# Optimization experiments

Hardware: AMD Instinct MI355X
Metric: run time of the kernel (lower is better)

Reference implementation:

```python
import jax, jax.numpy as jnp
import numpy as np

B, C, H, W, K = 16, 64, 256, 256, 3

def setup_inputs() -> dict:
    key = jax.random.key(0)
    ks = jax.random.split(key, 3)
    x = jax.random.normal(ks[0], (B, C, H, W), dtype=jnp.float32)
    # ReDistribution params
    rd_k = jnp.ones((1, C, 1, 1), jnp.float32)
    rd_b = jnp.zeros((1, C, 1, 1), jnp.float32)
    # Spectral binary activation beta
    beta = jnp.ones((1,), jnp.float32)
    # HardBinaryConv real-valued latent weights (Conv2d default init scale)
    fan_in = C * K * K
    bound = 1.0 / np.sqrt(fan_in)
    conv_w = jax.random.uniform(ks[1], (C, C, K, K), jnp.float32, -bound, bound)
    # RPReLU params
    pr_bias0 = jnp.zeros((1, C, 1, 1), jnp.float32)
    prelu_w = jnp.full((C,), 0.25, jnp.float32)
    pr_bias1 = jnp.zeros((1, C, 1, 1), jnp.float32)
    return {"x": x, "rd_k": rd_k, "rd_b": rd_b, "beta": beta,
            "conv_w": conv_w, "pr_bias0": pr_bias0, "prelu_w": prelu_w,
            "pr_bias1": pr_bias1}

def _ste(hard, soft):
    # straight-through estimator: forward=hard, backward grads flow via soft
    return jax.lax.stop_gradient(hard - soft) + soft

def reference(x, rd_k, rd_b, beta, conv_w, pr_bias0, prelu_w, pr_bias1):
    sg = jax.lax.stop_gradient
    # ReDistribution
    out = x * rd_k + rd_b
    # Spectral binary activation with tanh STE
    out = _ste(jnp.sign(out), jnp.tanh(out * beta))
    # HardBinaryConv: per-output-channel mean |w| scaling, sign binarize, clip STE
    scaling = sg(jnp.mean(jnp.abs(conv_w), axis=(1, 2, 3), keepdims=True))  # [C,1,1,1]
    bw = _ste(scaling * jnp.sign(conv_w), jnp.clip(conv_w, -1.0, 1.0))
    y = jax.lax.conv_general_dilated(
        out, bw, window_strides=(1, 1), padding=((1, 1), (1, 1)),
        dimension_numbers=("NCHW", "OIHW", "NCHW"))
    # RPReLU: bias0 -> per-channel PReLU -> bias1
    y = y + pr_bias0
    y = jnp.where(y >= 0, y, prelu_w[None, :, None, None] * y)
    y = y + pr_bias1
    return y + x
```

## Files before the change

### kernel.cpp

```cpp
#include <hip/hip_runtime.h>
#include <cstdint>
#include <cstddef>

#define Bn 16
#define Cn 64
#define Hn 256
#define Wn 256
#define HWn (Hn * Wn)
#define PIX (Bn * HWn)

#define TH 8
#define TW 64
#define NBLK (Wn / TW * Hn / TH * Bn)

__global__ __launch_bounds__(64) void pack_weights(const float* __restrict__ w,
                                                   const float* __restrict__ b0g,
                                                   const float* __restrict__ pwg,
                                                   const float* __restrict__ b1g,
                                                   uint64_t* __restrict__ wbits,
                                                   float4* __restrict__ par,
                                                   int* __restrict__ corr) {
    const int co = blockIdx.x;
    const int ci = threadIdx.x;
    const float* wp = w + ((size_t)co * Cn + ci) * 9;
    float v[9];
    float asum = 0.f;
    #pragma unroll
    for (int t = 0; t < 9; ++t) { v[t] = wp[t]; asum += fabsf(v[t]); }
    uint64_t m[9];
    #pragma unroll
    for (int t = 0; t < 9; ++t) m[t] = __ballot(v[t] > 0.f);
    #pragma unroll
    for (int off = 32; off; off >>= 1) asum += __shfl_xor(asum, off);
    if (ci == 0) {
        #pragma unroll
        for (int t = 0; t < 9; ++t) {
            wbits[co * 9 + t] = m[t];
            corr[co * 9 + t]  = 64 - 2 * (int)__popcll(m[t]);
        }
        par[co] = make_float4(asum * (1.f / (Cn * 9)), b0g[co], pwg[co], b1g[co]);
    }
}

__global__ __launch_bounds__(256, 4) void fused(const float* __restrict__ x,
                                                const float* __restrict__ rdk,
                                                const float* __restrict__ rdb,
                                                const uint64_t* __restrict__ wbits,
                                                const float4* __restrict__ par,
                                                const int* __restrict__ corr,
                                                float* __restrict__ out) {
    __shared__ uint64_t s_a[TH + 2][TW + 2];
    __shared__ float4 s_par[Cn];
    __shared__ float2 s_rd[Cn];

    const int tid = threadIdx.x;

    const int hw_id   = blockIdx.x;
    const int logical = (hw_id & 7) * (NBLK / 8) + (hw_id >> 3);
    const int w0 = (logical & 3) * TW;
    const int h0 = ((logical >> 2) & 31) * TH;
    const int n  = logical >> 7;

    if (tid < Cn) {
        s_par[tid] = par[tid];
        s_rd[tid]  = make_float2(rdk[tid], rdb[tid]);
    }
    __syncthreads();

    const float* xn = x + (size_t)n * Cn * HWn;
    for (int task = tid; task < 340; task += 256) {
        if (task < 320) {
            const int r  = task >> 5;
            const int pp = task & 31;
            const int gh = h0 - 1 + r;
            const int gw = w0 + pp * 2;
            uint64_t b0 = 0, b1 = 0;
            if (gh >= 0 && gh < Hn) {
                const float* xp = xn + (size_t)gh * Wn + gw;
                #pragma unroll 8
                for (int ci = 0; ci < Cn; ++ci) {
                    const float2 v = *reinterpret_cast<const float2*>(xp + (size_t)ci * HWn);
                    const float2 kb = s_rd[ci];
                    const uint64_t bit = 1ull << ci;
                    if (fmaf(v.x, kb.x, kb.y) > 0.f) b0 |= bit;
                    if (fmaf(v.y, kb.x, kb.y) > 0.f) b1 |= bit;
                }
            }
            s_a[r][1 + 2 * pp] = b0;
            s_a[r][2 + 2 * pp] = b1;
        } else {
            const int t2 = task - 320;
            const int r = t2 >> 1;
            const int side = t2 & 1;
            const int gh = h0 - 1 + r;
            const int gw = side ? (w0 + TW) : (w0 - 1);
            uint64_t b = 0;
            if (gh >= 0 && gh < Hn && gw >= 0 && gw < Wn) {
                const float* xp = xn + (size_t)gh * Wn + gw;
                #pragma unroll 8
                for (int ci = 0; ci < Cn; ++ci) {
                    const float v = xp[(size_t)ci * HWn];
                    const float2 kb = s_rd[ci];
                    if (fmaf(v, kb.x, kb.y) > 0.f) b |= 1ull << ci;
                }
            }
            s_a[r][side ? (TW + 1) : 0] = b;
        }
    }
    __syncthreads();

    const int lane = tid & 63;
    const int co_base = __builtin_amdgcn_readfirstlane((tid >> 6) * 16);
    const int w = w0 + lane;
    const unsigned cmask = (w == 0) ? 0x49u : (w == Wn - 1 ? 0x124u : 0u);
    const int any_edge = (w0 == 0) | (w0 + TW == Wn) | (h0 == 0) | (h0 + TH == Hn);

    uint64_t A[TH + 2][3];
    #pragma unroll
    for (int r = 0; r < TH + 2; ++r)
        #pragma unroll
        for (int dw = 0; dw < 3; ++dw)
            A[r][dw] = s_a[r][lane + dw];

    const size_t base_n = (size_t)n * Cn * HWn + (size_t)h0 * Wn + w;

    for (int c2 = 0; c2 < 8; ++c2) {
        const int coA = co_base + c2 * 2;
        const uint64_t* wbp = wbits + (size_t)coA * 9;
        uint64_t wba[9], wbb[9];
        #pragma unroll
        for (int t = 0; t < 9; ++t) { wba[t] = wbp[t]; wbb[t] = wbp[9 + t]; }
        const float4 pA = s_par[coA];
        const float4 pB = s_par[coA + 1];

        const float* xpc = x + base_n + (size_t)coA * HWn;
        float* opc = out + base_n + (size_t)coA * HWn;
        float xv[16];
        #pragma unroll
        for (int j = 0; j < 2; ++j)
            #pragma unroll
            for (int rr = 0; rr < TH; ++rr)
                xv[j * 8 + rr] = xpc[(size_t)j * HWn + (size_t)rr * Wn];

        #pragma unroll
        for (int r = 0; r < TH; ++r) {
            int accA = 0, accB = 0;
            #pragma unroll
            for (int dh = 0; dh < 3; ++dh)
                #pragma unroll
                for (int dw = 0; dw < 3; ++dw) {
                    accA += (int)__popcll(A[r + dh][dw] ^ wba[dh * 3 + dw]);
                    accB += (int)__popcll(A[r + dh][dw] ^ wbb[dh * 3 + dw]);
                }
            int isumA = 576 - 2 * accA;
            int isumB = 576 - 2 * accB;

            if (any_edge) {
                const int h = h0 + r;
                const unsigned imask = cmask |
                    ((h == 0) ? 0x7u : (h == Hn - 1 ? 0x1C0u : 0u));
                if (__any((int)imask)) {
                    #pragma unroll
                    for (int t = 0; t < 9; ++t)
                        if (imask & (1u << t)) {
                            isumA -= corr[coA * 9 + t];
                            isumB -= corr[(coA + 1) * 9 + t];
                        }
                }
            }

            float yA = fmaf(pA.x, (float)isumA, pA.y);
            yA = (yA >= 0.f) ? yA : yA * pA.z;
            yA += pA.w;
            float yB = fmaf(pB.x, (float)isumB, pB.y);
            yB = (yB >= 0.f) ? yB : yB * pB.z;
            yB += pB.w;
            opc[(size_t)r * Wn]       = yA + xv[r];
            opc[HWn + (size_t)r * Wn] = yB + xv[8 + r];
        }
    }
}

extern "C" void kernel_launch(void* const* d_in, const int* in_sizes, int n_in,
                              void* d_out, int out_size, void* d_ws, size_t ws_size,
                              hipStream_t stream) {
    const float* x      = (const float*)d_in[0];
    const float* rd_k   = (const float*)d_in[1];
    const float* rd_b   = (const float*)d_in[2];
    const float* conv_w = (const float*)d_in[4];
    const float* pb0    = (const float*)d_in[5];
    const float* pw     = (const float*)d_in[6];
    const float* pb1    = (const float*)d_in[7];
    float* out = (float*)d_out;

    uint8_t* ws = (uint8_t*)d_ws;
    uint64_t* wbits = (uint64_t*)ws;
    float4*   par   = (float4*)(ws + 4608);
    int*      corr  = (int*)(ws + 4608 + 1024);

    pack_weights<<<Cn, 64, 0, stream>>>(conv_w, pb0, pw, pb1, wbits, par, corr);
    fused<<<NBLK, 256, 0, stream>>>(x, rd_k, rd_b, wbits, par, corr, out);
}
```

Before: 199.8 us.

## Replace XNOR-popcount binary conv with int8 MFMA on ±1 activations

The binarized activations are now staged in shared memory as ±1 int8 vectors per pixel, with zero padding at image borders and an XOR swizzle to avoid bank conflicts. The weights are expanded to ±1 int8 fragments. The 3x3 convolution is computed with `mfma_i32_16x16x64_i8` instead of scalar XOR/popcount loops, which also removes the border-correction table. The aim is to move the bit-counting ALU work onto matrix cores. In exchange it uses more shared memory (about 42KB, with the occupancy hint lowered from 4 to 3 blocks) and stores outputs in narrower 16-pixel segments per channel.

New measurement: 202.4 us. About the same (+1.3%).

```diff
diff --git a/kernel.cpp b/kernel.cpp
--- a/kernel.cpp
+++ b/kernel.cpp
@@ -7,19 +7,20 @@
 #define Hn 256
 #define Wn 256
 #define HWn (Hn * Wn)
-#define PIX (Bn * HWn)
-
 #define TH 8
 #define TW 64
+#define ROWS (TH + 2)
+#define COLS (TW + 2)
 #define NBLK (Wn / TW * Hn / TH * Bn)
+
+typedef int i32x4 __attribute__((ext_vector_type(4)));
 
 __global__ __launch_bounds__(64) void pack_weights(const float* __restrict__ w,
                                                    const float* __restrict__ b0g,
                                                    const float* __restrict__ pwg,
                                                    const float* __restrict__ b1g,
                                                    uint64_t* __restrict__ wbits,
-                                                   float4* __restrict__ par,
-                                                   int* __restrict__ corr) {
+                                                   float4* __restrict__ par) {
     const int co = blockIdx.x;
     const int ci = threadIdx.x;
     const float* wp = w + ((size_t)co * Cn + ci) * 9;
@@ -34,22 +35,18 @@
     for (int off = 32; off; off >>= 1) asum += __shfl_xor(asum, off);
     if (ci == 0) {
         #pragma unroll
-        for (int t = 0; t < 9; ++t) {
-            wbits[co * 9 + t] = m[t];
-            corr[co * 9 + t]  = 64 - 2 * (int)__popcll(m[t]);
-        }
+        for (int t = 0; t < 9; ++t) wbits[co * 9 + t] = m[t];
         par[co] = make_float4(asum * (1.f / (Cn * 9)), b0g[co], pwg[co], b1g[co]);
     }
 }
 
-__global__ __launch_bounds__(256, 4) void fused(const float* __restrict__ x,
+__global__ __launch_bounds__(256, 3) void fused(const float* __restrict__ x,
                                                 const float* __restrict__ rdk,
                                                 const float* __restrict__ rdb,
                                                 const uint64_t* __restrict__ wbits,
                                                 const float4* __restrict__ par,
-                                                const int* __restrict__ corr,
                                                 float* __restrict__ out) {
-    __shared__ uint64_t s_a[TH + 2][TW + 2];
+    __shared__ __align__(16) signed char s_act[ROWS * COLS * 64];
     __shared__ float4 s_par[Cn];
     __shared__ float2 s_rd[Cn];
 
@@ -68,115 +65,102 @@
     __syncthreads();
 
     const float* xn = x + (size_t)n * Cn * HWn;
-    for (int task = tid; task < 340; task += 256) {
-        if (task < 320) {
-            const int r  = task >> 5;
-            const int pp = task & 31;
-            const int gh = h0 - 1 + r;
-            const int gw = w0 + pp * 2;
-            uint64_t b0 = 0, b1 = 0;
-            if (gh >= 0 && gh < Hn) {
-                const float* xp = xn + (size_t)gh * Wn + gw;
-                #pragma unroll 8
-                for (int ci = 0; ci < Cn; ++ci) {
-                    const float2 v = *reinterpret_cast<const float2*>(xp + (size_t)ci * HWn);
-                    const float2 kb = s_rd[ci];
-                    const uint64_t bit = 1ull << ci;
-                    if (fmaf(v.x, kb.x, kb.y) > 0.f) b0 |= bit;
-                    if (fmaf(v.y, kb.x, kb.y) > 0.f) b1 |= bit;
+    for (int pix = tid; pix < ROWS * COLS; pix += 256) {
+        const int r = pix / COLS;
+        const int c = pix - r * COLS;
+        const int gh = h0 - 1 + r, gw = w0 - 1 + c;
+        signed char* dst = s_act + pix * 64;
+        if (gh >= 0 && gh < Hn && gw >= 0 && gw < Wn) {
+            const float* xp = xn + (size_t)gh * Wn + gw;
+            #pragma unroll
+            for (int g = 0; g < 4; ++g) {
+                unsigned wd[4];
+                #pragma unroll
+                for (int q = 0; q < 4; ++q) {
+                    unsigned v = 0;
+                    #pragma unroll
+                    for (int b = 0; b < 4; ++b) {
+                        const int ci = g * 16 + q * 4 + b;
+                        const float2 kb = s_rd[ci];
+                        const float a = fmaf(xp[(size_t)ci * HWn], kb.x, kb.y);
+                        v |= (unsigned)(unsigned char)(a > 0.f ? 1 : -1) << (8 * b);
+                    }
+                    wd[q] = v;
                 }
+                i32x4 t = {(int)wd[0], (int)wd[1], (int)wd[2], (int)wd[3]};
+                *(i32x4*)(dst + ((g ^ (c & 3)) * 16)) = t;
             }
-            s_a[r][1 + 2 * pp] = b0;
-            s_a[r][2 + 2 * pp] = b1;
         } else {
-            const int t2 = task - 320;
-            const int r = t2 >> 1;
-            const int side = t2 & 1;
-            const int gh = h0 - 1 + r;
-            const int gw = side ? (w0 + TW) : (w0 - 1);
-            uint64_t b = 0;
-            if (gh >= 0 && gh < Hn && gw >= 0 && gw < Wn) {
-                const float* xp = xn + (size_t)gh * Wn + gw;
-                #pragma unroll 8
-                for (int ci = 0; ci < Cn; ++ci) {
-                    const float v = xp[(size_t)ci * HWn];
-                    const float2 kb = s_rd[ci];
-                    if (fmaf(v, kb.x, kb.y) > 0.f) b |= 1ull << ci;
-                }
-            }
-            s_a[r][side ? (TW + 1) : 0] = b;
+            const i32x4 z = {0, 0, 0, 0};
+            #pragma unroll
+            for (int g = 0; g < 4; ++g) *(i32x4*)(dst + g * 16) = z;
         }
     }
     __syncthreads();
 
     const int lane = tid & 63;
-    const int co_base = __builtin_amdgcn_readfirstlane((tid >> 6) * 16);
-    const int w = w0 + lane;
-    const unsigned cmask = (w == 0) ? 0x49u : (w == Wn - 1 ? 0x124u : 0u);
-    const int any_edge = (w0 == 0) | (w0 + TW == Wn) | (h0 == 0) | (h0 + TH == Hn);
+    const int g    = lane >> 4;
+    const int ln   = lane & 15;
+    const int cobase = (tid >> 6) * 16;
 
-    uint64_t A[TH + 2][3];
+    i32x4 afr[9];
+    {
+        const uint64_t* wbp = wbits + (size_t)(cobase + ln) * 9;
+        #pragma unroll
+        for (int t = 0; t < 9; ++t) {
+            const unsigned slice = (unsigned)(wbp[t] >> (g * 16)) & 0xFFFFu;
+            unsigned wq[4];
+            #pragma unroll
+            for (int q = 0; q < 4; ++q) {
+                unsigned v = 0;
+                #pragma unroll
+                for (int b = 0; b < 4; ++b)
+                    v |= (unsigned)(unsigned char)(((slice >> (q * 4 + b)) & 1) ? 1 : -1)
+                         << (8 * b);
+                wq[q] = v;
+            }
+            i32x4 t4 = {(int)wq[0], (int)wq[1], (int)wq[2], (int)wq[3]};
+            afr[t] = t4;
+        }
+    }
+
+    const int co_out0 = cobase + g * 4;
+    float4 pj[4];
     #pragma unroll
-    for (int r = 0; r < TH + 2; ++r)
+    for (int j = 0; j < 4; ++j) pj[j] = s_par[co_out0 + j];
+
+    int swz[3];
+    #pragma unroll
+    for (int dw = 0; dw < 3; ++dw) swz[dw] = (g ^ ((dw + ln) & 3)) * 16;
+
+    const size_t obase0 = ((size_t)(n * Cn + co_out0)) * HWn
+                        + (size_t)h0 * Wn + w0 + ln;
+
+    #pragma unroll 2
+    for (int nt = 0; nt < 32; ++nt) {
+        const int r  = nt >> 2;
+        const int wc = (nt & 3) * 16;
+        i32x4 acc = {0, 0, 0, 0};
         #pragma unroll
-        for (int dw = 0; dw < 3; ++dw)
-            A[r][dw] = s_a[r][lane + dw];
-
-    const size_t base_n = (size_t)n * Cn * HWn + (size_t)h0 * Wn + w;
-
-    for (int c2 = 0; c2 < 8; ++c2) {
-        const int coA = co_base + c2 * 2;
-        const uint64_t* wbp = wbits + (size_t)coA * 9;
-        uint64_t wba[9], wbb[9];
+        for (int dh = 0; dh < 3; ++dh) {
+            const int rowb = (r + dh) * COLS;
+            #pragma unroll
+            for (int dw = 0; dw < 3; ++dw) {
+                const int c = wc + dw + ln;
+                const i32x4 bfr = *(const i32x4*)(s_act + (rowb + c) * 64 + swz[dw]);
+                acc = __builtin_amdgcn_mfma_i32_16x16x64_i8(afr[dh * 3 + dw], bfr,
+                                                            acc, 0, 0, 0);
+            }
+        }
+        const size_t po = obase0 + (size_t)r * Wn + wc;
         #pragma unroll
-        for (int t = 0; t < 9; ++t) { wba[t] = wbp[t]; wbb[t] = wbp[9 + t]; }
-        const float4 pA = s_par[coA];
-        const float4 pB = s_par[coA + 1];
-
-        const float* xpc = x + base_n + (size_t)coA * HWn;
-        float* opc = out + base_n + (size_t)coA * HWn;
-        float xv[16];
-        #pragma unroll
-        for (int j = 0; j < 2; ++j)
-            #pragma unroll
-            for (int rr = 0; rr < TH; ++rr)
-                xv[j * 8 + rr] = xpc[(size_t)j * HWn + (size_t)rr * Wn];
-
-        #pragma unroll
-        for (int r = 0; r < TH; ++r) {
-            int accA = 0, accB = 0;
-            #pragma unroll
-            for (int dh = 0; dh < 3; ++dh)
-                #pragma unroll
-                for (int dw = 0; dw < 3; ++dw) {
-                    accA += (int)__popcll(A[r + dh][dw] ^ wba[dh * 3 + dw]);
-                    accB += (int)__popcll(A[r + dh][dw] ^ wbb[dh * 3 + dw]);
-                }
-            int isumA = 576 - 2 * accA;
-            int isumB = 576 - 2 * accB;
-
-            if (any_edge) {
-                const int h = h0 + r;
-                const unsigned imask = cmask |
-                    ((h == 0) ? 0x7u : (h == Hn - 1 ? 0x1C0u : 0u));
-                if (__any((int)imask)) {
-                    #pragma unroll
-                    for (int t = 0; t < 9; ++t)
-                        if (imask & (1u << t)) {
-                            isumA -= corr[coA * 9 + t];
-                            isumB -= corr[(coA + 1) * 9 + t];
-                        }
-                }
-            }
-
-            float yA = fmaf(pA.x, (float)isumA, pA.y);
-            yA = (yA >= 0.f) ? yA : yA * pA.z;
-            yA += pA.w;
-            float yB = fmaf(pB.x, (float)isumB, pB.y);
-            yB = (yB >= 0.f) ? yB : yB * pB.z;
-            yB += pB.w;
-            opc[(size_t)r * Wn]       = yA + xv[r];
-            opc[HWn + (size_t)r * Wn] = yB + xv[8 + r];
+        for (int j = 0; j < 4; ++j) {
+            const float4 p = pj[j];
+            float y = fmaf(p.x, (float)acc[j], p.y);
+            y = (y >= 0.f) ? y : y * p.z;
+            y += p.w;
+            const size_t gi = po + (size_t)j * HWn;
+            out[gi] = y + x[gi];
         }
     }
 }
@@ -196,8 +180,7 @@
     uint8_t* ws = (uint8_t*)d_ws;
     uint64_t* wbits = (uint64_t*)ws;
     float4*   par   = (float4*)(ws + 4608);
-    int*      corr  = (int*)(ws + 4608 + 1024);
 
-    pack_weights<<<Cn, 64, 0, stream>>>(conv_w, pb0, pw, pb1, wbits, par, corr);
-    fused<<<NBLK, 256, 0, stream>>>(x, rd_k, rd_b, wbits, par, corr, out);
+    pack_weights<<<Cn, 64, 0, stream>>>(conv_w, pb0, pw, pb1, wbits, par);
+    fused<<<NBLK, 256, 0, stream>>>(x, rd_k, rd_b, wbits, par, out);
 }
```
